# Optimization experiments

Hardware: AMD Instinct MI355X
Metric: run time of the kernel (lower is better)

The kernel has to match this reference:

```python
import jax, jax.numpy as jnp
import numpy as np

B, N, D_IN = 16, 2048, 256
C, H = 32, 64          # num_capsules, dim_capsules
HEADS, KD = 4, 64      # attention heads, key_dim = dim_capsules
ROUTINGS = 3
EPS_SQ = 1e-7
LN_EPS = 1e-3


def squash(v, axis=-1):
    s2 = jnp.sum(jnp.square(v), axis=axis, keepdims=True)
    scale = s2 / (1.0 + s2) / jnp.sqrt(s2 + EPS_SQ)
    return scale * v


def setup_inputs() -> dict:
    key = jax.random.key(0)
    ks = jax.random.split(key, 10)
    # VarianceScaling(scale=2.0, fan_avg, uniform) for W
    fan_avg = (D_IN + H) / 2.0
    limit = float(np.sqrt(3.0 * 2.0 / fan_avg))
    W = jax.random.uniform(ks[0], (C, D_IN, H), minval=-limit, maxval=limit, dtype=jnp.float32)
    b_caps = jnp.zeros((C, H), jnp.float32)
    gamma = jnp.full((1,), 3.0, jnp.float32)
    x = jax.random.normal(ks[1], (B, N, D_IN), dtype=jnp.float32)
    def glorot(k, shape):
        fin, fout = shape[0], int(np.prod(shape[1:]))
        lim = float(np.sqrt(6.0 / (fin + fout)))
        return jax.random.uniform(k, shape, minval=-lim, maxval=lim, dtype=jnp.float32)
    Wq = glorot(ks[2], (H, HEADS, KD)); bq = jnp.zeros((HEADS, KD), jnp.float32)
    Wk = glorot(ks[3], (H, HEADS, KD)); bk = jnp.zeros((HEADS, KD), jnp.float32)
    Wv = glorot(ks[4], (H, HEADS, KD)); bv = jnp.zeros((HEADS, KD), jnp.float32)
    Wo = glorot(ks[5], (HEADS, KD, H)); bo = jnp.zeros((H,), jnp.float32)
    ln_gamma = jnp.ones((H,), jnp.float32)
    ln_beta = jnp.zeros((H,), jnp.float32)
    return dict(x=x, W=W, b_caps=b_caps, gamma=gamma,
                Wq=Wq, bq=bq, Wk=Wk, bk=bk, Wv=Wv, bv=bv, Wo=Wo, bo=bo,
                ln_gamma=ln_gamma, ln_beta=ln_beta)


def dynamic_routing(u_hat):
    # u_hat: [B, N, C, H]
    b = jnp.zeros(u_hat.shape[:3] + (1,), u_hat.dtype)
    v = None
    for i in range(ROUTINGS):
        c = jax.nn.softmax(b, axis=2)                      # [B,N,C,1]
        s = jnp.sum(c * u_hat, axis=1, keepdims=True)      # [B,1,C,H]
        v = squash(s, axis=-1)
        if i < ROUTINGS - 1:
            agreement = jnp.sum(u_hat * v, axis=-1, keepdims=True)
            b = b + agreement
    return jnp.squeeze(v, axis=1)                          # [B,C,H]


def mha_self(xq, Wq, bq, Wk, bk, Wv, bv, Wo, bo):
    # xq: [B, C, H]
    q = jnp.einsum('bch,hnk->bcnk', xq, Wq) + bq
    k = jnp.einsum('bch,hnk->bcnk', xq, Wk) + bk
    v = jnp.einsum('bch,hnk->bcnk', xq, Wv) + bv
    scores = jnp.einsum('bqnd,bknd->bnqk', q, k) / jnp.sqrt(jnp.asarray(KD, xq.dtype))
    attn = jax.nn.softmax(scores, axis=-1)
    ctx = jnp.einsum('bnqk,bknd->bqnd', attn, v)
    return jnp.einsum('bqnd,ndh->bqh', ctx, Wo) + bo


def reference(x, W, b_caps, gamma, Wq, bq, Wk, bk, Wv, bv, Wo, bo, ln_gamma, ln_beta):
    u_hat = jnp.einsum('bnd,cdh->bnch', x, W) + b_caps[None, None]  # [B,N,C,H]
    routed = dynamic_routing(u_hat)                                  # [B,C,H]
    attended = mha_self(routed, Wq, bq, Wk, bk, Wv, bv, Wo, bo)
    y = attended + routed
    mu = jnp.mean(y, axis=-1, keepdims=True)
    var = jnp.mean(jnp.square(y - mu), axis=-1, keepdims=True)
    routed = (y - mu) / jnp.sqrt(var + LN_EPS) * ln_gamma + ln_beta
    return squash(routed, axis=-1) * gamma
```

## Files before the change

kernel.cpp:

```cpp
#include <hip/hip_runtime.h>
#include <cstddef>

typedef _Float16 f16;
typedef __attribute__((ext_vector_type(8))) _Float16 f16x8;
typedef __attribute__((ext_vector_type(4))) float f32x4;

namespace {
constexpr int kB = 16;
constexpr int kN = 2048;
constexpr int kD = 256;
constexpr int kC = 32;
constexpr int kH = 64;
constexpr int kHeads = 4;
constexpr int kKD = 64;
constexpr int kChunks = 32;
constexpr int kRows = kN / kChunks;
constexpr int kXJ = 64;

constexpr size_t OFF_XPART = 0;
constexpr size_t OFF_V     = OFF_XPART + 262144;
constexpr size_t OFF_WV    = OFF_V + 32768;
constexpr size_t OFF_BV    = OFF_WV + 131072;
constexpr size_t OFF_Y     = OFF_BV + 512;
constexpr size_t OFF_CS    = OFF_Y + 131072;
constexpr size_t OFF_BAR   = OFF_CS + 512;
constexpr size_t OFF_CTX   = OFF_BAR + 393216;
constexpr size_t OFF_XF16  = OFF_CTX + 524288;
constexpr size_t OFF_WVH   = OFF_XF16 + 4194304;
constexpr size_t OFF_CSP   = OFF_WVH + 65536;
constexpr size_t OFF_YP    = OFF_CSP + 16384;
constexpr size_t WS_NEED_PARTIAL = (OFF_YP + 4194304) * sizeof(float);

struct SMemR {
  f16 xsT[kD][kRows + 8];
  float aL[kRows][kC + 4];
  f16 pT[kC][kRows + 8];
  float csL[8][kC];
  float yL[kD];
  float sL[4][kH];
  float vL[kH];
  float csLs;
};
struct SMemA {
  float rL[kC * kH];
  float qL[kC][kKD];
  float kL[kC][kKD + 1];
  float vL[kC][kKD];
  float sc[kC][kC + 1];
};
struct SMemF {
  float cL[kHeads * kKD];
  float sL[4][kH];
};
union SMemU { SMemR r; SMemA a; SMemF f; };
}

__device__ __forceinline__ void bbar(int* __restrict__ bar, int b, int target) {
  __syncthreads();
  if (threadIdx.x == 0) {
    __hip_atomic_fetch_add(&bar[b * 16], 1, __ATOMIC_RELEASE,
                           __HIP_MEMORY_SCOPE_AGENT);
    const int* addr = &bar[b * 16];
    int guard = 0;
    for (;;) {
      int vv;
      asm volatile("global_load_dword %0, %1, off sc0 sc1\n\t"
                   "s_waitcnt vmcnt(0)"
                   : "=v"(vv)
                   : "v"(addr)
                   : "memory");
      if (vv >= target) break;
      __builtin_amdgcn_s_sleep(1);
      if (++guard > (1 << 20)) break;
    }
    __builtin_amdgcn_fence(__ATOMIC_ACQUIRE, "agent");
  }
  __syncthreads();
}

template <int CW, int ACC, int WRV>
__device__ __forceinline__ void sv_tail(const float* __restrict__ W,
                                        const float* __restrict__ b_caps,
                                        SMemR& r, float* __restrict__ v,
                                        float* __restrict__ Wv, f16* __restrict__ wvh,
                                        float* __restrict__ bv, int b, int c, int t) {
  const int w = t >> 6, h = t & 63;
  const float* Wc = W + (size_t)c * kD * kH;
  {
    float acc = 0.f;
#pragma unroll 8
    for (int d = w * 64; d < (w + 1) * 64; ++d)
      acc = fmaf(r.yL[d], Wc[(size_t)d * kH + h], acc);
    r.sL[w][h] = acc;
  }
  __syncthreads();
  if (t < 64) {
    const float bch = b_caps[c * kH + h];
    float s = r.sL[0][h] + r.sL[1][h] + r.sL[2][h] + r.sL[3][h] + r.csLs * bch;
    float s2 = s * s;
#pragma unroll
    for (int off = 32; off; off >>= 1) s2 += __shfl_xor(s2, off, 64);
    const float scale = s2 / (1.f + s2) * rsqrtf(s2 + 1e-7f);
    const float vh = scale * s;
    if (WRV) v[((size_t)b * kC + c) * kH + h] = vh;
    r.vL[h] = vh;
    if (CW) {
      float bvp = bch * vh;
#pragma unroll
      for (int off = 32; off; off >>= 1) bvp += __shfl_xor(bvp, off, 64);
      if (h == 0) bv[b * kC + c] = ACC ? (bv[b * kC + c] + bvp) : bvp;
    }
  }
  __syncthreads();
  if (CW) {
    float acc = 0.f;
    const float* Wrow = Wc + (size_t)t * kH;
#pragma unroll 8
    for (int hh = 0; hh < kH; ++hh) acc = fmaf(Wrow[hh], r.vL[hh], acc);
    const size_t idx = ((size_t)b * kC + c) * kD + t;
    const float nv = ACC ? (Wv[idx] + acc) : acc;
    Wv[idx] = nv;
    wvh[idx] = (f16)nv;
  }
}

__device__ __forceinline__ void route_phase(SMemR& r, const f16x8* __restrict__ af,
                                            const f16* __restrict__ wvh,
                                            const float* __restrict__ bv,
                                            f16* __restrict__ yp, float* __restrict__ csp,
                                            int b, int chunk, int t) {
  const int lane = t & 63, w = t >> 6;
  const int l15 = lane & 15, q = lane >> 4;
  const float bvc = bv[b * kC + (t & 31)];

  f32x4 acc0 = {0.f, 0.f, 0.f, 0.f}, acc1 = {0.f, 0.f, 0.f, 0.f};
  {
    const f16x8* B0 = reinterpret_cast<const f16x8*>(
        wvh + ((size_t)(b * kC + l15)) * kD + q * 8);
    const f16x8* B1 = reinterpret_cast<const f16x8*>(
        wvh + ((size_t)(b * kC + 16 + l15)) * kD + q * 8);
#pragma unroll
    for (int ks = 0; ks < 8; ++ks) {
      acc0 = __builtin_amdgcn_mfma_f32_16x16x32_f16(af[ks], B0[ks * 4], acc0, 0, 0, 0);
      acc1 = __builtin_amdgcn_mfma_f32_16x16x32_f16(af[ks], B1[ks * 4], acc1, 0, 0, 0);
    }
  }
#pragma unroll
  for (int rr = 0; rr < 4; ++rr) {
    r.aL[w * 16 + q * 4 + rr][l15] = acc0[rr];
    r.aL[w * 16 + q * 4 + rr][16 + l15] = acc1[rr];
  }
  __syncthreads();

  const int c = t & 31, sg = t >> 5;
  float csreg = 0.f;
#pragma unroll
  for (int k = 0; k < 8; ++k) {
    const int rr = sg * 8 + k;
    float L = bvc + r.aL[rr][c];
    float m = L;
#pragma unroll
    for (int off = 16; off; off >>= 1) m = fmaxf(m, __shfl_xor(m, off, 64));
    const float e = __expf(L - m);
    float ssum = e;
#pragma unroll
    for (int off = 16; off; off >>= 1) ssum += __shfl_xor(ssum, off, 64);
    const float p = e / ssum;
    r.pT[c][rr] = (f16)p;
    csreg += p;
  }
  r.csL[sg][c] = csreg;
  __syncthreads();

  const int mt2 = w & 1;
  const int ntb = (w >> 1) * 8;
  const f16x8 a0 = *reinterpret_cast<const f16x8*>(&r.pT[mt2 * 16 + l15][q * 8]);
  const f16x8 a1 = *reinterpret_cast<const f16x8*>(&r.pT[mt2 * 16 + l15][32 + q * 8]);
  const int cap = mt2 * 16 + q * 4;
#pragma unroll
  for (int i = 0; i < 8; ++i) {
    const int d0 = (ntb + i) * 16;
    const f16x8 b0 = *reinterpret_cast<const f16x8*>(&r.xsT[d0 + l15][q * 8]);
    const f16x8 b1 = *reinterpret_cast<const f16x8*>(&r.xsT[d0 + l15][32 + q * 8]);
    f32x4 o = {0.f, 0.f, 0.f, 0.f};
    o = __builtin_amdgcn_mfma_f32_16x16x32_f16(a0, b0, o, 0, 0, 0);
    o = __builtin_amdgcn_mfma_f32_16x16x32_f16(a1, b1, o, 0, 0, 0);
    f16* dst = yp + (((size_t)(b * kChunks + chunk)) * kC + cap) * kD + d0 + l15;
#pragma unroll
    for (int rr = 0; rr < 4; ++rr) dst[(size_t)rr * kD] = (f16)o[rr];
  }
  if (t < 32) {
    float s = 0.f;
#pragma unroll
    for (int j = 0; j < 8; ++j) s += r.csL[j][t];
    csp[((size_t)b * kChunks + chunk) * kC + t] = s;
  }
}

__global__ __launch_bounds__(256, 2) void k_all(
    const float* __restrict__ x, const float* __restrict__ W,
    const float* __restrict__ b_caps, const float* __restrict__ gamma,
    const float* __restrict__ Wq, const float* __restrict__ bq,
    const float* __restrict__ Wk, const float* __restrict__ bk,
    const float* __restrict__ Wvp, const float* __restrict__ bvp,
    const float* __restrict__ Wo, const float* __restrict__ bo,
    const float* __restrict__ ln_g, const float* __restrict__ ln_b,
    float* __restrict__ out, float* __restrict__ ws) {
  float* xpart = ws + OFF_XPART;
  float* v     = ws + OFF_V;
  float* Wv    = ws + OFF_WV;
  float* bv    = ws + OFF_BV;
  int*   bar   = (int*)(ws + OFF_BAR);
  float* ctx   = ws + OFF_CTX;
  f16*   wvh   = (f16*)(ws + OFF_WVH);
  float* csp   = ws + OFF_CSP;
  f16*   yp    = (f16*)(ws + OFF_YP);

  const int b = blockIdx.x, chunk = blockIdx.y;
  const int t = threadIdx.x;
  const int lane = t & 63, w = t >> 6;
  const int l15 = lane & 15, q = lane >> 4;
  const int n0 = chunk * kRows;
  const int c = chunk;

  __shared__ __align__(16) SMemU sm;

  {
    const float* xc = x + ((size_t)b * kN + n0) * kD + t;
    float s = 0.f;
#pragma unroll 16
    for (int n = 0; n < kRows; ++n) s += xc[(size_t)n * kD];
    xpart[((size_t)b * kChunks + chunk) * kD + t] = s;
  }
  f16x8 af[8];
  {
    const int row = w * 16 + l15;
    const float* xr = x + ((size_t)(b * kN + n0 + row)) * kD + q * 8;
#pragma unroll
    for (int ks = 0; ks < 8; ++ks) {
      const f32x4* p = reinterpret_cast<const f32x4*>(xr + ks * 32);
      const f32x4 lo = p[0], hi = p[1];
      f16x8 a;
      a[0] = (f16)lo[0]; a[1] = (f16)lo[1]; a[2] = (f16)lo[2]; a[3] = (f16)lo[3];
      a[4] = (f16)hi[0]; a[5] = (f16)hi[1]; a[6] = (f16)hi[2]; a[7] = (f16)hi[3];
      af[ks] = a;
      const int dbase = ks * 32 + q * 8;
#pragma unroll
      for (int i = 0; i < 8; ++i) {
        const int ii = (i + 2 * q) & 7;
        sm.r.xsT[dbase + ii][row] = a[ii];
      }
    }
  }
  bbar(bar, b, 32 * 1);

  {
    float s = 0.f;
#pragma unroll 8
    for (int ch = 0; ch < kChunks; ++ch)
      s += xpart[((size_t)b * kChunks + ch) * kD + t];
    sm.r.yL[t] = s * (1.f / (float)kC);
    if (t == 0) sm.r.csLs = (float)kN / (float)kC;
  }
  __syncthreads();
  sv_tail<1, 0, 0>(W, b_caps, sm.r, v, Wv, wvh, bv, b, c, t);
  bbar(bar, b, 32 * 2);

  route_phase(sm.r, af, wvh, bv, yp, csp, b, chunk, t);
  bbar(bar, b, 32 * 3);

  {
    float s = 0.f;
#pragma unroll 8
    for (int ch = 0; ch < kChunks; ++ch)
      s += (float)yp[(((size_t)b * kChunks + ch) * kC + c) * kD + t];
    sm.r.yL[t] = s;
    if (t < 32) {
      float cs_ = csp[((size_t)b * kChunks + t) * kC + c];
#pragma unroll
      for (int off = 16; off; off >>= 1) cs_ += __shfl_xor(cs_, off, 64);
      if (t == 0) sm.r.csLs = cs_;
    }
  }
  __syncthreads();
  sv_tail<1, 1, 0>(W, b_caps, sm.r, v, Wv, wvh, bv, b, c, t);
  bbar(bar, b, 32 * 4);

  route_phase(sm.r, af, wvh, bv, yp, csp, b, chunk, t);
  bbar(bar, b, 32 * 5);

  {
    float s = 0.f;
#pragma unroll 8
    for (int ch = 0; ch < kChunks; ++ch)
      s += (float)yp[(((size_t)b * kChunks + ch) * kC + c) * kD + t];
    sm.r.yL[t] = s;
    if (t < 32) {
      float cs_ = csp[((size_t)b * kChunks + t) * kC + c];
#pragma unroll
      for (int off = 16; off; off >>= 1) cs_ += __shfl_xor(cs_, off, 64);
      if (t == 0) sm.r.csLs = cs_;
    }
  }
  __syncthreads();
  sv_tail<0, 0, 1>(W, b_caps, sm.r, v, Wv, wvh, bv, b, c, t);
  bbar(bar, b, 32 * 6);

  if (chunk < kHeads) {
    const int head = chunk;
    const int kk = t & 63;
#pragma unroll
    for (int i = 0; i < 8; ++i)
      sm.a.rL[t + 256 * i] = v[(size_t)b * kC * kH + t + 256 * i];
    __syncthreads();
    float aq[8], ak[8], av[8];
    const float bbq = bq[head * kKD + kk];
    const float bbk = bk[head * kKD + kk];
    const float bbv = bvp[head * kKD + kk];
#pragma unroll
    for (int i = 0; i < 8; ++i) { aq[i] = bbq; ak[i] = bbk; av[i] = bbv; }
#pragma unroll 4
    for (int hh = 0; hh < kH; ++hh) {
      const size_t widx = ((size_t)hh * kHeads + head) * kKD + kk;
      const float wq = Wq[widx];
      const float wk2 = Wk[widx];
      const float wv2 = Wvp[widx];
#pragma unroll
      for (int i = 0; i < 8; ++i) {
        const float rv = sm.a.rL[(w + 4 * i) * kH + hh];
        aq[i] = fmaf(rv, wq, aq[i]);
        ak[i] = fmaf(rv, wk2, ak[i]);
        av[i] = fmaf(rv, wv2, av[i]);
      }
    }
#pragma unroll
    for (int i = 0; i < 8; ++i) {
      const int cc = w + 4 * i;
      sm.a.qL[cc][kk] = aq[i];
      sm.a.kL[cc][kk] = ak[i];
      sm.a.vL[cc][kk] = av[i];
    }
    __syncthreads();
#pragma unroll
    for (int i = 0; i < 4; ++i) {
      const int e = t + 256 * i, qc = e >> 5, kc2 = e & 31;
      float s = 0.f;
#pragma unroll 8
      for (int d = 0; d < kKD; ++d) s = fmaf(sm.a.qL[qc][d], sm.a.kL[kc2][d], s);
      sm.a.sc[qc][kc2] = s * 0.125f;
    }
    __syncthreads();
    if (t < kC) {
      float m = -1e30f;
#pragma unroll
      for (int kc2 = 0; kc2 < kC; ++kc2) m = fmaxf(m, sm.a.sc[t][kc2]);
      float ssum = 0.f;
#pragma unroll
      for (int kc2 = 0; kc2 < kC; ++kc2) {
        const float e2 = __expf(sm.a.sc[t][kc2] - m);
        sm.a.sc[t][kc2] = e2;
        ssum += e2;
      }
      const float inv = 1.f / ssum;
#pragma unroll
      for (int kc2 = 0; kc2 < kC; ++kc2) sm.a.sc[t][kc2] *= inv;
    }
    __syncthreads();
#pragma unroll
    for (int i = 0; i < 8; ++i) {
      const int e = t + 256 * i, qc = e >> 6, d = e & 63;
      float s = 0.f;
#pragma unroll 8
      for (int kc2 = 0; kc2 < kC; ++kc2) s = fmaf(sm.a.sc[qc][kc2], sm.a.vL[kc2][d], s);
      ctx[(((size_t)b * kC + qc) * kHeads + head) * kKD + d] = s;
    }
  }
  bbar(bar, b, 32 * 7);

  {
    const int bc = b * kC + chunk;
    const int h = t & 63;
    sm.f.cL[t] = ctx[(size_t)bc * (kHeads * kKD) + t];
    __syncthreads();
    float acc = 0.f;
#pragma unroll 8
    for (int nd = w * 64; nd < (w + 1) * 64; ++nd)
      acc = fmaf(sm.f.cL[nd], Wo[(size_t)nd * kH + h], acc);
    sm.f.sL[w][h] = acc;
    __syncthreads();
    if (t < 64) {
      const float yv = sm.f.sL[0][h] + sm.f.sL[1][h] + sm.f.sL[2][h] + sm.f.sL[3][h] +
                       bo[h] + v[(size_t)bc * kH + h];
      float mu = yv;
#pragma unroll
      for (int off = 32; off; off >>= 1) mu += __shfl_xor(mu, off, 64);
      mu *= (1.f / (float)kH);
      const float dv = yv - mu;
      float var = dv * dv;
#pragma unroll
      for (int off = 32; off; off >>= 1) var += __shfl_xor(var, off, 64);
      var *= (1.f / (float)kH);
      const float nrm = dv * rsqrtf(var + 1e-3f) * ln_g[h] + ln_b[h];
      float s2 = nrm * nrm;
#pragma unroll
      for (int off = 32; off; off >>= 1) s2 += __shfl_xor(s2, off, 64);
      const float scale = s2 / (1.f + s2) * rsqrtf(s2 + 1e-7f);
      out[(size_t)bc * kH + h] = scale * nrm * gamma[0];
    }
  }
}


__global__ __launch_bounds__(256) void k_xpart(const float* __restrict__ x,
                                               float* __restrict__ xpart,
                                               f16* __restrict__ xh) {
  const int b = blockIdx.x, j = blockIdx.y, d = threadIdx.x;
  const size_t base = ((size_t)b * kN + (size_t)j * 32) * kD + d;
  const float* xp = x + base;
  f16* xo = xh + base;
  float s = 0.f;
#pragma unroll
  for (int n = 0; n < 32; ++n) {
    const float v = xp[(size_t)n * kD];
    s += v;
    xo[(size_t)n * kD] = (f16)v;
  }
  xpart[((size_t)b * kXJ + j) * kD + d] = s;
}

__global__ __launch_bounds__(256) void k_sv(
    const float* __restrict__ W, const float* __restrict__ b_caps,
    const float* __restrict__ xpart, const float* __restrict__ y,
    const float* __restrict__ csum, const f16* __restrict__ ypart,
    const float* __restrict__ cspart, float* __restrict__ v,
    float* __restrict__ Wv, f16* __restrict__ Wvh, float* __restrict__ bv,
    const int mode, const int computeWv, const int accWv, const int npart) {
  const int bc = blockIdx.x, b = bc >> 5, c = bc & 31;
  const int t = threadIdx.x;
  const int w = t >> 6, h = t & 63;
  __shared__ float yL[kD];
  __shared__ float sL[4][kH];
  __shared__ float vL[kH];
  __shared__ float csLs;

  if (mode == 0) {
    float s = 0.f;
#pragma unroll 8
    for (int j = 0; j < kXJ; ++j) s += xpart[((size_t)b * kXJ + j) * kD + t];
    yL[t] = s * (1.f / (float)kC);
    if (t == 0) csLs = (float)kN / (float)kC;
  } else if (npart > 0) {
    float s = 0.f;
#pragma unroll 8
    for (int ch = 0; ch < kChunks; ++ch)
      s += (float)ypart[(((size_t)b * kChunks + ch) * kC + c) * kD + t];
    yL[t] = s;
    if (t < 32) {
      float cs_ = cspart[((size_t)b * kChunks + t) * kC + c];
#pragma unroll
      for (int off = 16; off; off >>= 1) cs_ += __shfl_xor(cs_, off, 64);
      if (t == 0) csLs = cs_;
    }
  } else {
    yL[t] = y[(size_t)bc * kD + t];
    if (t == 0) csLs = csum[bc];
  }
  __syncthreads();

  const float* Wc = W + (size_t)c * kD * kH;
  {
    float acc = 0.f;
#pragma unroll 8
    for (int d = w * 64; d < (w + 1) * 64; ++d)
      acc = fmaf(yL[d], Wc[(size_t)d * kH + h], acc);
    sL[w][h] = acc;
  }
  __syncthreads();

  if (t < 64) {
    const float bch = b_caps[c * kH + h];
    float s = sL[0][h] + sL[1][h] + sL[2][h] + sL[3][h] + csLs * bch;
    float s2 = s * s;
#pragma unroll
    for (int off = 32; off; off >>= 1) s2 += __shfl_xor(s2, off, 64);
    const float scale = s2 / (1.f + s2) * rsqrtf(s2 + 1e-7f);
    const float vh = scale * s;
    v[(size_t)bc * kH + h] = vh;
    vL[h] = vh;
    if (computeWv) {
      float bvp = bch * vh;
#pragma unroll
      for (int off = 32; off; off >>= 1) bvp += __shfl_xor(bvp, off, 64);
      if (h == 0) bv[bc] = accWv ? (bv[bc] + bvp) : bvp;
    }
  }
  __syncthreads();
  if (computeWv) {
    float acc = 0.f;
    const float* Wrow = Wc + (size_t)t * kH;
#pragma unroll 8
    for (int hh = 0; hh < kH; ++hh) acc = fmaf(Wrow[hh], vL[hh], acc);
    const size_t idx = (size_t)bc * kD + t;
    const float nv = accWv ? (Wv[idx] + acc) : acc;
    Wv[idx] = nv;
    Wvh[idx] = (f16)nv;
  }
}

__global__ __launch_bounds__(256) void k_route(
    const f16* __restrict__ xh, const f16* __restrict__ Wvh,
    const float* __restrict__ bv, float* __restrict__ y,
    float* __restrict__ csum, f16* __restrict__ ypart,
    float* __restrict__ cspart, const int usePart) {
  const int b = blockIdx.x, chunk = blockIdx.y;
  const int t = threadIdx.x;
  const int lane = t & 63, w = t >> 6;
  const int l15 = lane & 15, q = lane >> 4;

  __shared__ __align__(16) f16 xsT[kD][kRows + 8];
  __shared__ float aL[kRows][kC + 4];
  __shared__ __align__(16) f16 pT[kC][kRows + 8];
  __shared__ float csL[8][kC];

  const int n0 = chunk * kRows;
  const float bvc = bv[b * kC + (t & 31)];

  f32x4 acc0 = {0.f, 0.f, 0.f, 0.f}, acc1 = {0.f, 0.f, 0.f, 0.f};
  {
    const int row = w * 16 + l15;
    const f16x8* Ar = reinterpret_cast<const f16x8*>(
        xh + ((size_t)(b * kN + n0 + row)) * kD + q * 8);
    const f16x8* B0 = reinterpret_cast<const f16x8*>(
        Wvh + ((size_t)(b * kC + l15)) * kD + q * 8);
    const f16x8* B1 = reinterpret_cast<const f16x8*>(
        Wvh + ((size_t)(b * kC + 16 + l15)) * kD + q * 8);
#pragma unroll
    for (int ks = 0; ks < 8; ++ks) {
      f16x8 af = Ar[ks * 4];
      acc0 = __builtin_amdgcn_mfma_f32_16x16x32_f16(af, B0[ks * 4], acc0, 0, 0, 0);
      acc1 = __builtin_amdgcn_mfma_f32_16x16x32_f16(af, B1[ks * 4], acc1, 0, 0, 0);
      const int dbase = ks * 32 + q * 8;
#pragma unroll
      for (int i = 0; i < 8; ++i) {
        const int ii = (i + 2 * q) & 7;
        xsT[dbase + ii][row] = af[ii];
      }
    }
  }
#pragma unroll
  for (int r = 0; r < 4; ++r) {
    aL[w * 16 + q * 4 + r][l15] = acc0[r];
    aL[w * 16 + q * 4 + r][16 + l15] = acc1[r];
  }
  __syncthreads();

  const int c = t & 31, sg = t >> 5;
  float csreg = 0.f;
#pragma unroll
  for (int k = 0; k < 8; ++k) {
    const int r = sg * 8 + k;
    float L = bvc + aL[r][c];
    float m = L;
#pragma unroll
    for (int off = 16; off; off >>= 1) m = fmaxf(m, __shfl_xor(m, off, 64));
    const float e = __expf(L - m);
    float ssum = e;
#pragma unroll
    for (int off = 16; off; off >>= 1) ssum += __shfl_xor(ssum, off, 64);
    const float p = e / ssum;
    pT[c][r] = (f16)p;
    csreg += p;
  }
  csL[sg][c] = csreg;
  __syncthreads();

  const int mt2 = w & 1;
  const int ntb = (w >> 1) * 8;
  const f16x8 a0 = *reinterpret_cast<const f16x8*>(&pT[mt2 * 16 + l15][q * 8]);
  const f16x8 a1 = *reinterpret_cast<const f16x8*>(&pT[mt2 * 16 + l15][32 + q * 8]);
  const int cap = mt2 * 16 + q * 4;
#pragma unroll
  for (int i = 0; i < 8; ++i) {
    const int d0 = (ntb + i) * 16;
    const f16x8 b0 = *reinterpret_cast<const f16x8*>(&xsT[d0 + l15][q * 8]);
    const f16x8 b1 = *reinterpret_cast<const f16x8*>(&xsT[d0 + l15][32 + q * 8]);
    f32x4 o = {0.f, 0.f, 0.f, 0.f};
    o = __builtin_amdgcn_mfma_f32_16x16x32_f16(a0, b0, o, 0, 0, 0);
    o = __builtin_amdgcn_mfma_f32_16x16x32_f16(a1, b1, o, 0, 0, 0);
    if (usePart) {
      f16* dst = ypart + (((size_t)(b * kChunks + chunk)) * kC + cap) * kD + d0 + l15;
#pragma unroll
      for (int r = 0; r < 4; ++r) dst[(size_t)r * kD] = (f16)o[r];
    } else {
      float* dst = y + ((size_t)(b * kC + cap)) * kD + d0 + l15;
#pragma unroll
      for (int r = 0; r < 4; ++r) atomicAdd(dst + (size_t)r * kD, o[r]);
    }
  }
  if (t < 32) {
    float s = 0.f;
#pragma unroll
    for (int j = 0; j < 8; ++j) s += csL[j][t];
    if (usePart) cspart[((size_t)b * kChunks + chunk) * kC + t] = s;
    else atomicAdd(csum + b * kC + t, s);
  }
}

__global__ __launch_bounds__(256) void k_attn(
    const float* __restrict__ routed,
    const float* __restrict__ Wq, const float* __restrict__ bq,
    const float* __restrict__ Wk, const float* __restrict__ bk,
    const float* __restrict__ Wvp, const float* __restrict__ bvp,
    float* __restrict__ ctx) {
  const int b = blockIdx.x, head = blockIdx.y, t = threadIdx.x;
  const int kk = t & 63, w = t >> 6;
  __shared__ float rL[kC * kH];
  __shared__ float qL[kC][kKD];
  __shared__ float kL[kC][kKD + 1];
  __shared__ float vL[kC][kKD];
  __shared__ float sc[kC][kC + 1];
#pragma unroll
  for (int i = 0; i < 8; ++i) rL[t + 256 * i] = routed[(size_t)b * kC * kH + t + 256 * i];
  __syncthreads();
  float aq[8], ak[8], av[8];
  const float bbq = bq[head * kKD + kk];
  const float bbk = bk[head * kKD + kk];
  const float bbv = bvp[head * kKD + kk];
#pragma unroll
  for (int i = 0; i < 8; ++i) { aq[i] = bbq; ak[i] = bbk; av[i] = bbv; }
#pragma unroll 4
  for (int hh = 0; hh < kH; ++hh) {
    const size_t widx = ((size_t)hh * kHeads + head) * kKD + kk;
    const float wq = Wq[widx];
    const float wk2 = Wk[widx];
    const float wv2 = Wvp[widx];
#pragma unroll
    for (int i = 0; i < 8; ++i) {
      const float r = rL[(w + 4 * i) * kH + hh];
      aq[i] = fmaf(r, wq, aq[i]);
      ak[i] = fmaf(r, wk2, ak[i]);
      av[i] = fmaf(r, wv2, av[i]);
    }
  }
#pragma unroll
  for (int i = 0; i < 8; ++i) {
    const int cc = w + 4 * i;
    qL[cc][kk] = aq[i];
    kL[cc][kk] = ak[i];
    vL[cc][kk] = av[i];
  }
  __syncthreads();
#pragma unroll
  for (int i = 0; i < 4; ++i) {
    const int e = t + 256 * i, qc = e >> 5, kc2 = e & 31;
    float s = 0.f;
#pragma unroll 8
    for (int d = 0; d < kKD; ++d) s = fmaf(qL[qc][d], kL[kc2][d], s);
    sc[qc][kc2] = s * 0.125f;
  }
  __syncthreads();
  if (t < kC) {
    float m = -1e30f;
#pragma unroll
    for (int kc2 = 0; kc2 < kC; ++kc2) m = fmaxf(m, sc[t][kc2]);
    float ssum = 0.f;
#pragma unroll
    for (int kc2 = 0; kc2 < kC; ++kc2) {
      const float e2 = __expf(sc[t][kc2] - m);
      sc[t][kc2] = e2;
      ssum += e2;
    }
    const float inv = 1.f / ssum;
#pragma unroll
    for (int kc2 = 0; kc2 < kC; ++kc2) sc[t][kc2] *= inv;
  }
  __syncthreads();
#pragma unroll
  for (int i = 0; i < 8; ++i) {
    const int e = t + 256 * i, qc = e >> 6, d = e & 63;
    float s = 0.f;
#pragma unroll 8
    for (int kc2 = 0; kc2 < kC; ++kc2) s = fmaf(sc[qc][kc2], vL[kc2][d], s);
    ctx[(((size_t)b * kC + qc) * kHeads + head) * kKD + d] = s;
  }
}

__global__ __launch_bounds__(256) void k_final(
    const float* __restrict__ ctx, const float* __restrict__ Wo,
    const float* __restrict__ bo, const float* __restrict__ routed,
    const float* __restrict__ ln_g, const float* __restrict__ ln_b,
    const float* __restrict__ gamma, float* __restrict__ out) {
  const int bc = blockIdx.x, t = threadIdx.x;
  const int w = t >> 6, h = t & 63;
  __shared__ float cL[kHeads * kKD];
  __shared__ float sL[4][kH];
  cL[t] = ctx[(size_t)bc * (kHeads * kKD) + t];
  __syncthreads();
  float acc = 0.f;
#pragma unroll 8
  for (int nd = w * 64; nd < (w + 1) * 64; ++nd)
    acc = fmaf(cL[nd], Wo[(size_t)nd * kH + h], acc);
  sL[w][h] = acc;
  __syncthreads();
  if (t < 64) {
    const float yv = sL[0][h] + sL[1][h] + sL[2][h] + sL[3][h] + bo[h] +
                     routed[(size_t)bc * kH + h];
    float mu = yv;
#pragma unroll
    for (int off = 32; off; off >>= 1) mu += __shfl_xor(mu, off, 64);
    mu *= (1.f / (float)kH);
    const float dv = yv - mu;
    float var = dv * dv;
#pragma unroll
    for (int off = 32; off; off >>= 1) var += __shfl_xor(var, off, 64);
    var *= (1.f / (float)kH);
    const float nrm = dv * rsqrtf(var + 1e-3f) * ln_g[h] + ln_b[h];
    float s2 = nrm * nrm;
#pragma unroll
    for (int off = 32; off; off >>= 1) s2 += __shfl_xor(s2, off, 64);
    const float scale = s2 / (1.f + s2) * rsqrtf(s2 + 1e-7f);
    out[(size_t)bc * kH + h] = scale * nrm * gamma[0];
  }
}

extern "C" void kernel_launch(void* const* d_in, const int* in_sizes, int n_in,
                              void* d_out, int out_size, void* d_ws, size_t ws_size,
                              hipStream_t stream) {
  (void)in_sizes; (void)n_in; (void)out_size;
  const float* x      = (const float*)d_in[0];
  const float* W      = (const float*)d_in[1];
  const float* b_caps = (const float*)d_in[2];
  const float* gamma  = (const float*)d_in[3];
  const float* Wq     = (const float*)d_in[4];
  const float* bq     = (const float*)d_in[5];
  const float* Wk     = (const float*)d_in[6];
  const float* bk     = (const float*)d_in[7];
  const float* Wv_in  = (const float*)d_in[8];
  const float* bv_in  = (const float*)d_in[9];
  const float* Wo     = (const float*)d_in[10];
  const float* bo     = (const float*)d_in[11];
  const float* ln_g   = (const float*)d_in[12];
  const float* ln_b   = (const float*)d_in[13];
  float* out = (float*)d_out;
  float* ws  = (float*)d_ws;

  static int s_ok = -1;
  if (s_ok < 0) {
    int dev = 0;
    hipGetDevice(&dev);
    hipDeviceProp_t prop{};
    hipGetDeviceProperties(&prop, dev);
    int occ = 0;
    hipError_t e = hipOccupancyMaxActiveBlocksPerMultiprocessor(&occ, k_all, 256, 0);
    s_ok = (e == hipSuccess &&
            (long long)occ * prop.multiProcessorCount >= (long long)kB * kChunks)
               ? 1 : 0;
  }

  if (s_ok && ws_size >= WS_NEED_PARTIAL) {
    hipMemsetAsync((void*)(ws + OFF_BAR), 0, kB * 16 * sizeof(int), stream);
    k_all<<<dim3(kB, kChunks), 256, 0, stream>>>(
        x, W, b_caps, gamma, Wq, bq, Wk, bk, Wv_in, bv_in, Wo, bo, ln_g, ln_b,
        out, ws);
    return;
  }

  float* xpart = ws + OFF_XPART;
  float* v     = ws + OFF_V;
  float* Wv    = ws + OFF_WV;
  float* bv    = ws + OFF_BV;
  float* y     = ws + OFF_Y;
  float* cs    = ws + OFF_CS;
  float* ctx   = ws + OFF_CTX;
  f16*   xf16  = (f16*)(ws + OFF_XF16);
  f16*   wvh   = (f16*)(ws + OFF_WVH);
  float* csp   = ws + OFF_CSP;
  f16*   yp    = (f16*)(ws + OFF_YP);

  const int usePart = (ws_size >= WS_NEED_PARTIAL) ? 1 : 0;

  k_xpart<<<dim3(kB, kXJ), 256, 0, stream>>>(x, xpart, xf16);
  k_sv<<<kB * kC, 256, 0, stream>>>(W, b_caps, xpart, y, cs, yp, csp, v, Wv, wvh, bv,
                                    0, 1, 0, 0);
  if (!usePart) {
    hipMemsetAsync(y, 0, (size_t)kB * kC * kD * sizeof(float), stream);
    hipMemsetAsync(cs, 0, (size_t)kB * kC * sizeof(float), stream);
  }
  k_route<<<dim3(kB, kChunks), 256, 0, stream>>>(xf16, wvh, bv, y, cs, yp, csp, usePart);
  k_sv<<<kB * kC, 256, 0, stream>>>(W, b_caps, xpart, y, cs, yp, csp, v, Wv, wvh, bv,
                                    1, 1, 1, usePart ? kChunks : 0);
  if (!usePart) {
    hipMemsetAsync(y, 0, (size_t)kB * kC * kD * sizeof(float), stream);
    hipMemsetAsync(cs, 0, (size_t)kB * kC * sizeof(float), stream);
  }
  k_route<<<dim3(kB, kChunks), 256, 0, stream>>>(xf16, wvh, bv, y, cs, yp, csp, usePart);
  k_sv<<<kB * kC, 256, 0, stream>>>(W, b_caps, xpart, y, cs, yp, csp, v, Wv, wvh, bv,
                                    1, 0, 0, usePart ? kChunks : 0);
  k_attn<<<dim3(kB, kHeads), 256, 0, stream>>>(v, Wq, bq, Wk, bk, Wv_in, bv_in, ctx);
  k_final<<<kB * kC, 256, 0, stream>>>(ctx, Wo, bo, v, ln_g, ln_b, gamma, out);
}
```

Measured before the change: 174.0 us.

## Replace grid barrier fences with cache-bypassing loads/stores for cross-block data

Cross-block shared buffers (partials, Wv half copies, bv, v, ctx) are now written and read with sc0 sc1 global instructions that bypass the non-coherent caches. This lets the grid barrier drop its release atomic and acquire fence, which flush or invalidate caches. Partial-sum reads are also batched so all loads issue before a single vmcnt wait. The risk is a coherence bug if any cross-block access still goes through the normal cached path (for example the fp32 Wv read-modify-write in sv_tail), and uncached accesses may have higher latency.

```diff
diff --git a/kernel.cpp b/kernel.cpp
--- a/kernel.cpp
+++ b/kernel.cpp
@@ -55,11 +55,38 @@
 union SMemU { SMemR r; SMemA a; SMemF f; };
 }
 
+__device__ __forceinline__ void issue_ld_f32(float& d, const float* p) {
+  asm volatile("global_load_dword %0, %1, off sc0 sc1" : "=v"(d) : "v"(p));
+}
+__device__ __forceinline__ void issue_ld_u16(unsigned int& d, const f16* p) {
+  asm volatile("global_load_ushort %0, %1, off sc0 sc1" : "=v"(d) : "v"(p));
+}
+__device__ __forceinline__ void issue_ld_b128(f16x8& d, const f16* p) {
+  asm volatile("global_load_dwordx4 %0, %1, off sc0 sc1" : "=v"(d) : "v"(p));
+}
+__device__ __forceinline__ void wait_vm0() {
+  asm volatile("s_waitcnt vmcnt(0)" ::: "memory");
+  __builtin_amdgcn_sched_barrier(0);
+}
+__device__ __forceinline__ float ld_f32_uc(const float* p) {
+  float d;
+  issue_ld_f32(d, p);
+  wait_vm0();
+  return d;
+}
+__device__ __forceinline__ void st_f32_uc(float* p, float v) {
+  asm volatile("global_store_dword %0, %1, off sc0 sc1" :: "v"(p), "v"(v) : "memory");
+}
+__device__ __forceinline__ void st_f16_uc(f16* p, f16 v) {
+  unsigned int u = (unsigned int)__builtin_bit_cast(unsigned short, v);
+  asm volatile("global_store_short %0, %1, off sc0 sc1" :: "v"(p), "v"(u) : "memory");
+}
+
 __device__ __forceinline__ void bbar(int* __restrict__ bar, int b, int target) {
+  asm volatile("s_waitcnt vmcnt(0)" ::: "memory");
   __syncthreads();
   if (threadIdx.x == 0) {
-    __hip_atomic_fetch_add(&bar[b * 16], 1, __ATOMIC_RELEASE,
-                           __HIP_MEMORY_SCOPE_AGENT);
+    atomicAdd(&bar[b * 16], 1);
     const int* addr = &bar[b * 16];
     int guard = 0;
     for (;;) {
@@ -73,7 +100,6 @@
       __builtin_amdgcn_s_sleep(1);
       if (++guard > (1 << 20)) break;
     }
-    __builtin_amdgcn_fence(__ATOMIC_ACQUIRE, "agent");
   }
   __syncthreads();
 }
@@ -102,13 +128,17 @@
     for (int off = 32; off; off >>= 1) s2 += __shfl_xor(s2, off, 64);
     const float scale = s2 / (1.f + s2) * rsqrtf(s2 + 1e-7f);
     const float vh = scale * s;
-    if (WRV) v[((size_t)b * kC + c) * kH + h] = vh;
+    if (WRV) st_f32_uc(v + ((size_t)b * kC + c) * kH + h, vh);
     r.vL[h] = vh;
     if (CW) {
       float bvp = bch * vh;
 #pragma unroll
       for (int off = 32; off; off >>= 1) bvp += __shfl_xor(bvp, off, 64);
-      if (h == 0) bv[b * kC + c] = ACC ? (bv[b * kC + c] + bvp) : bvp;
+      if (h == 0) {
+        float nbv = bvp;
+        if (ACC) nbv += ld_f32_uc(bv + b * kC + c);
+        st_f32_uc(bv + b * kC + c, nbv);
+      }
     }
   }
   __syncthreads();
@@ -120,7 +150,30 @@
     const size_t idx = ((size_t)b * kC + c) * kD + t;
     const float nv = ACC ? (Wv[idx] + acc) : acc;
     Wv[idx] = nv;
-    wvh[idx] = (f16)nv;
+    st_f16_uc(wvh + idx, (f16)nv);
+  }
+}
+
+__device__ __forceinline__ void load_partials(SMemR& r, const f16* __restrict__ yp,
+                                              const float* __restrict__ csp,
+                                              int b, int c, int t) {
+  unsigned int tmp[kChunks];
+  const f16* ypp = yp + ((size_t)b * kChunks * kC + c) * kD + t;
+#pragma unroll
+  for (int ch = 0; ch < kChunks; ++ch)
+    issue_ld_u16(tmp[ch], ypp + (size_t)ch * kC * kD);
+  float csv = 0.f;
+  if (t < 32) issue_ld_f32(csv, csp + ((size_t)b * kChunks + t) * kC + c);
+  wait_vm0();
+  float s = 0.f;
+#pragma unroll
+  for (int ch = 0; ch < kChunks; ++ch)
+    s += (float)__builtin_bit_cast(f16, (unsigned short)tmp[ch]);
+  r.yL[t] = s;
+  if (t < 32) {
+#pragma unroll
+    for (int off = 16; off; off >>= 1) csv += __shfl_xor(csv, off, 64);
+    if (t == 0) r.csLs = csv;
   }
 }
 
@@ -131,18 +184,23 @@
                                             int b, int chunk, int t) {
   const int lane = t & 63, w = t >> 6;
   const int l15 = lane & 15, q = lane >> 4;
-  const float bvc = bv[b * kC + (t & 31)];
+  const float bvc = ld_f32_uc(bv + b * kC + (t & 31));
 
   f32x4 acc0 = {0.f, 0.f, 0.f, 0.f}, acc1 = {0.f, 0.f, 0.f, 0.f};
   {
-    const f16x8* B0 = reinterpret_cast<const f16x8*>(
-        wvh + ((size_t)(b * kC + l15)) * kD + q * 8);
-    const f16x8* B1 = reinterpret_cast<const f16x8*>(
-        wvh + ((size_t)(b * kC + 16 + l15)) * kD + q * 8);
+    f16x8 b0f[8], b1f[8];
+    const f16* w0 = wvh + ((size_t)(b * kC + l15)) * kD + q * 8;
+    const f16* w1 = wvh + ((size_t)(b * kC + 16 + l15)) * kD + q * 8;
 #pragma unroll
     for (int ks = 0; ks < 8; ++ks) {
-      acc0 = __builtin_amdgcn_mfma_f32_16x16x32_f16(af[ks], B0[ks * 4], acc0, 0, 0, 0);
-      acc1 = __builtin_amdgcn_mfma_f32_16x16x32_f16(af[ks], B1[ks * 4], acc1, 0, 0, 0);
+      issue_ld_b128(b0f[ks], w0 + ks * 32);
+      issue_ld_b128(b1f[ks], w1 + ks * 32);
+    }
+    wait_vm0();
+#pragma unroll
+    for (int ks = 0; ks < 8; ++ks) {
+      acc0 = __builtin_amdgcn_mfma_f32_16x16x32_f16(af[ks], b0f[ks], acc0, 0, 0, 0);
+      acc1 = __builtin_amdgcn_mfma_f32_16x16x32_f16(af[ks], b1f[ks], acc1, 0, 0, 0);
     }
   }
 #pragma unroll
@@ -187,13 +245,13 @@
     o = __builtin_amdgcn_mfma_f32_16x16x32_f16(a1, b1, o, 0, 0, 0);
     f16* dst = yp + (((size_t)(b * kChunks + chunk)) * kC + cap) * kD + d0 + l15;
 #pragma unroll
-    for (int rr = 0; rr < 4; ++rr) dst[(size_t)rr * kD] = (f16)o[rr];
+    for (int rr = 0; rr < 4; ++rr) st_f16_uc(dst + (size_t)rr * kD, (f16)o[rr]);
   }
   if (t < 32) {
     float s = 0.f;
 #pragma unroll
     for (int j = 0; j < 8; ++j) s += r.csL[j][t];
-    csp[((size_t)b * kChunks + chunk) * kC + t] = s;
+    st_f32_uc(csp + ((size_t)b * kChunks + chunk) * kC + t, s);
   }
 }
 
@@ -230,7 +288,7 @@
     float s = 0.f;
 #pragma unroll 16
     for (int n = 0; n < kRows; ++n) s += xc[(size_t)n * kD];
-    xpart[((size_t)b * kChunks + chunk) * kD + t] = s;
+    st_f32_uc(xpart + ((size_t)b * kChunks + chunk) * kD + t, s);
   }
   f16x8 af[8];
   {
@@ -255,10 +313,15 @@
   bbar(bar, b, 32 * 1);
 
   {
+    float tmp[kChunks];
+    const float* xpp = xpart + (size_t)b * kChunks * kD + t;
+#pragma unroll
+    for (int ch = 0; ch < kChunks; ++ch)
+      issue_ld_f32(tmp[ch], xpp + (size_t)ch * kD);
+    wait_vm0();
     float s = 0.f;
-#pragma unroll 8
-    for (int ch = 0; ch < kChunks; ++ch)
-      s += xpart[((size_t)b * kChunks + ch) * kD + t];
+#pragma unroll
+    for (int ch = 0; ch < kChunks; ++ch) s += tmp[ch];
     sm.r.yL[t] = s * (1.f / (float)kC);
     if (t == 0) sm.r.csLs = (float)kN / (float)kC;
   }
@@ -269,19 +332,7 @@
   route_phase(sm.r, af, wvh, bv, yp, csp, b, chunk, t);
   bbar(bar, b, 32 * 3);
 
-  {
-    float s = 0.f;
-#pragma unroll 8
-    for (int ch = 0; ch < kChunks; ++ch)
-      s += (float)yp[(((size_t)b * kChunks + ch) * kC + c) * kD + t];
-    sm.r.yL[t] = s;
-    if (t < 32) {
-      float cs_ = csp[((size_t)b * kChunks + t) * kC + c];
-#pragma unroll
-      for (int off = 16; off; off >>= 1) cs_ += __shfl_xor(cs_, off, 64);
-      if (t == 0) sm.r.csLs = cs_;
-    }
-  }
+  load_partials(sm.r, yp, csp, b, c, t);
   __syncthreads();
   sv_tail<1, 1, 0>(W, b_caps, sm.r, v, Wv, wvh, bv, b, c, t);
   bbar(bar, b, 32 * 4);
@@ -289,19 +340,7 @@
   route_phase(sm.r, af, wvh, bv, yp, csp, b, chunk, t);
   bbar(bar, b, 32 * 5);
 
-  {
-    float s = 0.f;
-#pragma unroll 8
-    for (int ch = 0; ch < kChunks; ++ch)
-      s += (float)yp[(((size_t)b * kChunks + ch) * kC + c) * kD + t];
-    sm.r.yL[t] = s;
-    if (t < 32) {
-      float cs_ = csp[((size_t)b * kChunks + t) * kC + c];
-#pragma unroll
-      for (int off = 16; off; off >>= 1) cs_ += __shfl_xor(cs_, off, 64);
-      if (t == 0) sm.r.csLs = cs_;
-    }
-  }
+  load_partials(sm.r, yp, csp, b, c, t);
   __syncthreads();
   sv_tail<0, 0, 1>(W, b_caps, sm.r, v, Wv, wvh, bv, b, c, t);
   bbar(bar, b, 32 * 6);
@@ -309,9 +348,15 @@
   if (chunk < kHeads) {
     const int head = chunk;
     const int kk = t & 63;
-#pragma unroll
-    for (int i = 0; i < 8; ++i)
-      sm.a.rL[t + 256 * i] = v[(size_t)b * kC * kH + t + 256 * i];
+    {
+      float tmp[8];
+#pragma unroll
+      for (int i = 0; i < 8; ++i)
+        issue_ld_f32(tmp[i], v + (size_t)b * kC * kH + t + 256 * i);
+      wait_vm0();
+#pragma unroll
+      for (int i = 0; i < 8; ++i) sm.a.rL[t + 256 * i] = tmp[i];
+    }
     __syncthreads();
     float aq[8], ak[8], av[8];
     const float bbq = bq[head * kKD + kk];
@@ -372,7 +417,7 @@
       float s = 0.f;
 #pragma unroll 8
       for (int kc2 = 0; kc2 < kC; ++kc2) s = fmaf(sm.a.sc[qc][kc2], sm.a.vL[kc2][d], s);
-      ctx[(((size_t)b * kC + qc) * kHeads + head) * kKD + d] = s;
+      st_f32_uc(ctx + (((size_t)b * kC + qc) * kHeads + head) * kKD + d, s);
     }
   }
   bbar(bar, b, 32 * 7);
@@ -380,7 +425,12 @@
   {
     const int bc = b * kC + chunk;
     const int h = t & 63;
-    sm.f.cL[t] = ctx[(size_t)bc * (kHeads * kKD) + t];
+    float ctmp;
+    issue_ld_f32(ctmp, ctx + (size_t)bc * (kHeads * kKD) + t);
+    float vtmp = 0.f;
+    if (t < 64) issue_ld_f32(vtmp, v + (size_t)bc * kH + h);
+    wait_vm0();
+    sm.f.cL[t] = ctmp;
     __syncthreads();
     float acc = 0.f;
 #pragma unroll 8
@@ -390,7 +440,7 @@
     __syncthreads();
     if (t < 64) {
       const float yv = sm.f.sL[0][h] + sm.f.sL[1][h] + sm.f.sL[2][h] + sm.f.sL[3][h] +
-                       bo[h] + v[(size_t)bc * kH + h];
+                       bo[h] + vtmp;
       float mu = yv;
 #pragma unroll
       for (int off = 32; off; off >>= 1) mu += __shfl_xor(mu, off, 64);
```

Measured after the change: 174.6 us. No clear change (+0.3%).
